# Kernel tuning notes

Measured on AMD Instinct MI355X. Metric: run time of the kernel, lower is better.

Reference implementation:

```python
import jax, jax.numpy as jnp
import numpy as np

DIM = 1024
N_HEAD = 16
N_KV_HEAD = 4
HEAD_DIM = DIM // N_HEAD  # 64
INTER = 2688
B, N = 2, 2048
EPS = 1e-6


def setup_inputs() -> dict:
    key = jax.random.key(0)
    ks = jax.random.split(key, 10)
    std = 0.02
    x = jax.random.normal(ks[0], (B, N, DIM), dtype=jnp.float32)
    # rotary embedding: theta = pos * 10000^(-2i/d), cos/sin of shape [N, HEAD_DIM//2]
    inv_freq = 1.0 / (10000.0 ** (np.arange(0, HEAD_DIM, 2, dtype=np.float32) / HEAD_DIM))
    t = np.arange(N, dtype=np.float32)
    ang = np.outer(t, inv_freq)  # [N, HEAD_DIM//2]
    rope_cos = jnp.asarray(np.cos(ang))
    rope_sin = jnp.asarray(np.sin(ang))
    mask = jnp.tril(jnp.ones((N, N), dtype=bool))  # True = attend
    return {
        "x": x,
        "w_attn_norm": jnp.ones((DIM,), jnp.float32),
        "w_ffn_norm": jnp.ones((DIM,), jnp.float32),
        "Wq": jax.random.normal(ks[1], (DIM, N_HEAD * HEAD_DIM), jnp.float32) * std,
        "Wkv": jax.random.normal(ks[2], (DIM, 2 * N_KV_HEAD * HEAD_DIM), jnp.float32) * std,
        "Wo": jax.random.normal(ks[3], (N_HEAD * HEAD_DIM, DIM), jnp.float32) * std,
        "W1": jax.random.normal(ks[4], (DIM, INTER), jnp.float32) * std,
        "W2": jax.random.normal(ks[5], (INTER, DIM), jnp.float32) * std,
        "W3": jax.random.normal(ks[6], (DIM, INTER), jnp.float32) * std,
        "rope_cos": rope_cos,
        "rope_sin": rope_sin,
        "mask": mask,
    }


def _rms_norm(x, w):
    # nn.functional.rms_norm: x / sqrt(mean(x^2) + eps) * w
    return x * jax.lax.rsqrt(jnp.mean(x * x, axis=-1, keepdims=True) + EPS) * w


def _apply_rope(x, cos, sin):
    # x: [b, n, h, d]; consecutive pairs (x[2k], x[2k+1]) form complex numbers
    xr = x[..., 0::2]
    xi = x[..., 1::2]
    c = cos[None, :, None, :]
    s = sin[None, :, None, :]
    yr = xr * c - xi * s
    yi = xr * s + xi * c
    return jnp.stack([yr, yi], axis=-1).reshape(x.shape)


def _block(x, w_attn_norm, w_ffn_norm, Wq, Wkv, Wo, W1, W2, W3, rope_cos, rope_sin, mask):
    b, n, _ = x.shape
    # --- attention (GQA, use_cache=False prefill) ---
    h = _rms_norm(x, w_attn_norm)
    q = (h @ Wq).reshape(b, n, N_HEAD, HEAD_DIM)
    kv = h @ Wkv
    k, v = jnp.split(kv, 2, axis=-1)
    k = k.reshape(b, n, N_KV_HEAD, HEAD_DIM)
    v = v.reshape(b, n, N_KV_HEAD, HEAD_DIM)
    q = _apply_rope(q, rope_cos, rope_sin)
    k = _apply_rope(k, rope_cos, rope_sin)
    # einops repeat 'b n h d -> b n (r h) d' == tile along head axis
    r = N_HEAD // N_KV_HEAD
    k = jnp.tile(k, (1, 1, r, 1))
    v = jnp.tile(v, (1, 1, r, 1))
    scale = HEAD_DIM ** -0.5
    scores = jnp.einsum('bnhd,bmhd->bhnm', q, k) * scale
    scores = jnp.where(mask[None, None, :, :], scores, jnp.finfo(scores.dtype).min)
    attn = jax.nn.softmax(scores, axis=-1)
    o = jnp.einsum('bhnm,bmhd->bnhd', attn, v).reshape(b, n, N_HEAD * HEAD_DIM)
    x = x + o @ Wo
    # --- SwiGLU MLP ---
    h2 = _rms_norm(x, w_ffn_norm)
    ff = (jax.nn.silu(h2 @ W1) * (h2 @ W3)) @ W2
    return x + ff


def reference(x, w_attn_norm, w_ffn_norm, Wq, Wkv, Wo, W1, W2, W3, rope_cos, rope_sin, mask):
    return _block(x, w_attn_norm, w_ffn_norm, Wq, Wkv, Wo, W1, W2, W3, rope_cos, rope_sin, mask)
```

## Files before the change

kernel.cpp:

```cpp
#include <hip/hip_runtime.h>

#define DIM 1024
#define NH 16
#define NKV 4
#define HD 64
#define INTER 2688
#define BB 2
#define NN 2048
#define MM (BB*NN)

typedef __attribute__((ext_vector_type(4))) float f32x4;
typedef __attribute__((ext_vector_type(16))) float f32x16;
typedef __attribute__((ext_vector_type(8))) short short8;

#define CROW(r,h) ((((r)&3)) + 8*((r)>>2) + 4*(h))

__device__ __forceinline__ unsigned short f2bf(float f) {
  union { float f; unsigned u; } v; v.f = f;
  unsigned r = v.u + 0x7fffu + ((v.u >> 16) & 1u);
  return (unsigned short)(r >> 16);
}

__device__ __forceinline__ void glds16(const unsigned short* g, unsigned short* l) {
  __builtin_amdgcn_global_load_lds(
      (const __attribute__((address_space(1))) void*)g,
      (__attribute__((address_space(3))) void*)l, 16, 0, 0);
}

__global__ void transpose_k(const float* __restrict__ W, unsigned short* __restrict__ Wt,
                            int K, int Nc) {
  __shared__ float tile[32][33];
  int n0 = blockIdx.x * 32, k0 = blockIdx.y * 32;
  int tx = threadIdx.x & 31, ty = threadIdx.x >> 5;
#pragma unroll
  for (int i = 0; i < 32; i += 8)
    tile[ty + i][tx] = W[(size_t)(k0 + ty + i) * Nc + n0 + tx];
  __syncthreads();
#pragma unroll
  for (int i = 0; i < 32; i += 8)
    Wt[(size_t)(n0 + ty + i) * K + k0 + tx] = f2bf(tile[tx][ty + i]);
}

__global__ void rmsnorm_k(const float* __restrict__ x, const float* __restrict__ w,
                          unsigned short* __restrict__ h) {
  int row = blockIdx.x;
  int t = threadIdx.x;
  const float4* xr = (const float4*)(x + (size_t)row * DIM);
  float4 v = xr[t];
  float ss = v.x * v.x + v.y * v.y + v.z * v.z + v.w * v.w;
#pragma unroll
  for (int o = 1; o < 64; o <<= 1) ss += __shfl_xor(ss, o);
  __shared__ float ps[4];
  if ((t & 63) == 0) ps[t >> 6] = ss;
  __syncthreads();
  float r = rsqrtf((ps[0] + ps[1] + ps[2] + ps[3]) * (1.0f / DIM) + 1e-6f);
  const float4* wr = (const float4*)w;
  float4 wv = wr[t];
  ushort4 o4;
  o4.x = f2bf(v.x * r * wv.x);
  o4.y = f2bf(v.y * r * wv.y);
  o4.z = f2bf(v.z * r * wv.z);
  o4.w = f2bf(v.w * r * wv.w);
  *(ushort4*)(h + (size_t)row * DIM + t * 4) = o4;
}

template <bool RES>
__global__ __launch_bounds__(256, 3) void gemm_f32(
    const unsigned short* __restrict__ A, const unsigned short* __restrict__ Bt,
    const float* __restrict__ res, float* __restrict__ C, int Nc, int K) {
  __shared__ __align__(16) unsigned short Asm[2 * 128 * 32];
  __shared__ __align__(16) unsigned short Bsm[2 * 128 * 32];
  int tid = threadIdx.x;
  int w = tid >> 6, l = tid & 63;
  int bm = blockIdx.y * 128, bn = blockIdx.x * 128;
  int wr = (w >> 1) * 64, wc = (w & 1) * 64;
  int c0 = l & 15, g = l >> 4;

  int sr = w * 32 + (l >> 2);
  int sc = ((l & 3) ^ ((sr >> 1) & 3)) * 8;
  const unsigned short* gA0 = A + (size_t)(bm + sr) * K + sc;
  const unsigned short* gA1 = A + (size_t)(bm + sr + 16) * K + sc;
  const unsigned short* gB0 = Bt + (size_t)(bn + sr) * K + sc;
  const unsigned short* gB1 = Bt + (size_t)(bn + sr + 16) * K + sc;
  int ls0 = (w * 32) * 32, ls1 = (w * 32 + 16) * 32;

  int aoff[4], boff[4];
#pragma unroll
  for (int m = 0; m < 4; m++) {
    int ra = wr + m * 16 + c0;
    aoff[m] = ra * 32 + (g ^ ((ra >> 1) & 3)) * 8;
    int rb = wc + m * 16 + c0;
    boff[m] = rb * 32 + (g ^ ((rb >> 1) & 3)) * 8;
  }

  f32x4 acc[4][4] = {};
  int nsteps = K / 32;
  glds16(gA0, &Asm[ls0]);
  glds16(gA1, &Asm[ls1]);
  glds16(gB0, &Bsm[ls0]);
  glds16(gB1, &Bsm[ls1]);
  __syncthreads();
  int buf = 0;
  for (int s = 0; s < nsteps; ++s) {
    int nb = buf ^ 1;
    if (s + 1 < nsteps) {
      int ko = (s + 1) * 32;
      glds16(gA0 + ko, &Asm[nb * 4096 + ls0]);
      glds16(gA1 + ko, &Asm[nb * 4096 + ls1]);
      glds16(gB0 + ko, &Bsm[nb * 4096 + ls0]);
      glds16(gB1 + ko, &Bsm[nb * 4096 + ls1]);
    }
    const unsigned short* As = &Asm[buf * 4096];
    const unsigned short* Bs = &Bsm[buf * 4096];
    short8 af[4], bf[4];
#pragma unroll
    for (int m = 0; m < 4; m++) af[m] = *(const short8*)&As[aoff[m]];
#pragma unroll
    for (int n = 0; n < 4; n++) bf[n] = *(const short8*)&Bs[boff[n]];
#pragma unroll
    for (int m = 0; m < 4; m++)
#pragma unroll
      for (int n = 0; n < 4; n++)
        acc[m][n] = __builtin_amdgcn_mfma_f32_16x16x32_bf16(af[m], bf[n], acc[m][n], 0, 0, 0);
    __syncthreads();
    buf = nb;
  }
  int gq = l >> 4;
#pragma unroll
  for (int m = 0; m < 4; m++) {
#pragma unroll
    for (int i = 0; i < 4; i++) {
      int row = bm + wr + m * 16 + gq * 4 + i;
#pragma unroll
      for (int n = 0; n < 4; n++) {
        int col = bn + wc + n * 16 + c0;
        float v = acc[m][n][i];
        if (RES) v += res[(size_t)row * Nc + col];
        C[(size_t)row * Nc + col] = v;
      }
    }
  }
}

__global__ __launch_bounds__(256, 3) void gemm_ffn13(
    const unsigned short* __restrict__ A, const unsigned short* __restrict__ B1t,
    const unsigned short* __restrict__ B3t, unsigned short* __restrict__ G,
    int Nc, int K) {
  __shared__ __align__(16) unsigned short Asm[2 * 128 * 32];
  __shared__ __align__(16) unsigned short B1sm[2 * 64 * 32];
  __shared__ __align__(16) unsigned short B3sm[2 * 64 * 32];
  int tid = threadIdx.x;
  int w = tid >> 6, l = tid & 63;
  int bm = blockIdx.y * 128, bn = blockIdx.x * 64;
  int wr = (w >> 1) * 64, wc = (w & 1) * 32;
  int c0 = l & 15, g = l >> 4;

  int sr = w * 32 + (l >> 2);
  int sb = w * 16 + (l >> 2);
  int sc  = ((l & 3) ^ ((sr >> 1) & 3)) * 8;
  int scb = ((l & 3) ^ ((sb >> 1) & 3)) * 8;
  const unsigned short* gA0 = A + (size_t)(bm + sr) * K + sc;
  const unsigned short* gA1 = A + (size_t)(bm + sr + 16) * K + sc;
  const unsigned short* gB1 = B1t + (size_t)(bn + sb) * K + scb;
  const unsigned short* gB3 = B3t + (size_t)(bn + sb) * K + scb;
  int ls0 = (w * 32) * 32, ls1 = (w * 32 + 16) * 32, lsb = (w * 16) * 32;

  int aoff[4], boff[2];
#pragma unroll
  for (int m = 0; m < 4; m++) {
    int ra = wr + m * 16 + c0;
    aoff[m] = ra * 32 + (g ^ ((ra >> 1) & 3)) * 8;
  }
#pragma unroll
  for (int n = 0; n < 2; n++) {
    int rb = wc + n * 16 + c0;
    boff[n] = rb * 32 + (g ^ ((rb >> 1) & 3)) * 8;
  }

  f32x4 a1[4][2] = {};
  f32x4 a3[4][2] = {};
  int nsteps = K / 32;
  glds16(gA0, &Asm[ls0]);
  glds16(gA1, &Asm[ls1]);
  glds16(gB1, &B1sm[lsb]);
  glds16(gB3, &B3sm[lsb]);
  __syncthreads();
  int buf = 0;
  for (int s = 0; s < nsteps; ++s) {
    int nb = buf ^ 1;
    if (s + 1 < nsteps) {
      int ko = (s + 1) * 32;
      glds16(gA0 + ko, &Asm[nb * 4096 + ls0]);
      glds16(gA1 + ko, &Asm[nb * 4096 + ls1]);
      glds16(gB1 + ko, &B1sm[nb * 2048 + lsb]);
      glds16(gB3 + ko, &B3sm[nb * 2048 + lsb]);
    }
    const unsigned short* As = &Asm[buf * 4096];
    const unsigned short* B1s = &B1sm[buf * 2048];
    const unsigned short* B3s = &B3sm[buf * 2048];
    short8 af[4], b1f[2], b3f[2];
#pragma unroll
    for (int m = 0; m < 4; m++) af[m] = *(const short8*)&As[aoff[m]];
#pragma unroll
    for (int n = 0; n < 2; n++) {
      b1f[n] = *(const short8*)&B1s[boff[n]];
      b3f[n] = *(const short8*)&B3s[boff[n]];
    }
#pragma unroll
    for (int m = 0; m < 4; m++)
#pragma unroll
      for (int n = 0; n < 2; n++) {
        a1[m][n] = __builtin_amdgcn_mfma_f32_16x16x32_bf16(af[m], b1f[n], a1[m][n], 0, 0, 0);
        a3[m][n] = __builtin_amdgcn_mfma_f32_16x16x32_bf16(af[m], b3f[n], a3[m][n], 0, 0, 0);
      }
    __syncthreads();
    buf = nb;
  }
  int gq = l >> 4;
#pragma unroll
  for (int m = 0; m < 4; m++) {
#pragma unroll
    for (int i = 0; i < 4; i++) {
      int row = bm + wr + m * 16 + gq * 4 + i;
#pragma unroll
      for (int n = 0; n < 2; n++) {
        int col = bn + wc + n * 16 + c0;
        float x1 = a1[m][n][i], x3 = a3[m][n][i];
        float sg = x1 / (1.0f + __expf(-x1));
        G[(size_t)row * Nc + col] = f2bf(sg * x3);
      }
    }
  }
}

__global__ void prep_qkv(const float* __restrict__ qkv, const float* __restrict__ cosb,
                         const float* __restrict__ sinb, unsigned short* __restrict__ qb,
                         unsigned short* __restrict__ kb, unsigned short* __restrict__ vtb) {
  int n = blockIdx.x, b = blockIdx.y;
  int t = threadIdx.x;
  const float* row = qkv + ((size_t)b * NN + n) * 1536;
#pragma unroll
  for (int p = t; p < 512; p += 256) {
    int head = p >> 5, j = p & 31;
    float xr = row[head * 64 + 2 * j], xi = row[head * 64 + 2 * j + 1];
    float c = cosb[n * 32 + j], s = sinb[n * 32 + j];
    size_t o = (((size_t)(b * NH + head)) * NN + n) * 64 + 2 * j;
    qb[o] = f2bf((xr * c - xi * s) * 0.125f);
    qb[o + 1] = f2bf((xr * s + xi * c) * 0.125f);
  }
  if (t < 128) {
    int kvh = t >> 5, j = t & 31;
    float xr = row[1024 + kvh * 64 + 2 * j], xi = row[1024 + kvh * 64 + 2 * j + 1];
    float c = cosb[n * 32 + j], s = sinb[n * 32 + j];
    size_t o = (((size_t)(b * NKV + kvh)) * NN + n) * 64 + 2 * j;
    kb[o] = f2bf(xr * c - xi * s);
    kb[o + 1] = f2bf(xr * s + xi * c);
  }
  {
    int kvh = t >> 6, d = t & 63;
    float v = row[1280 + kvh * 64 + d];
    vtb[(((size_t)(b * NKV + kvh)) * 64 + d) * NN + n] = f2bf(v);
  }
}

__global__ __launch_bounds__(256, 3) void attn_k(
    const unsigned short* __restrict__ qg_, const unsigned short* __restrict__ kg_,
    const unsigned short* __restrict__ vg_, unsigned short* __restrict__ ob) {
  __shared__ __align__(16) unsigned short Ksm[2][64 * 64];
  __shared__ __align__(16) unsigned short Vsm[2][64 * 64];
  int qb = (blockIdx.z == 0) ? (int)blockIdx.x : ((int)gridDim.x - 1 - (int)blockIdx.x);
  int h = blockIdx.y, b = blockIdx.z;
  int kvh = h & 3;
  int tid = threadIdx.x, w = tid >> 6, l = tid & 63;
  int q5 = l & 31, hi = l >> 5;
  int qwbase = qb * 128 + w * 32;
  int qgl = qwbase + q5;

  const unsigned short* Kg = kg_ + ((size_t)(b * NKV + kvh)) * NN * 64;
  const unsigned short* Vg = vg_ + ((size_t)(b * NKV + kvh)) * 64 * NN;

  short8 qf[4];
  {
    const unsigned short* qrow = qg_ + (((size_t)(b * NH + h)) * NN + qgl) * 64 + hi * 8;
#pragma unroll
    for (int d = 0; d < 4; d++) qf[d] = *(const short8*)(qrow + d * 16);
  }

  int srow = l >> 3;
  int schunk = (l & 7) ^ (srow & 7);
  const unsigned short* gK = Kg + (size_t)(w * 16 + srow) * 64 + schunk * 8;
  const unsigned short* gV = Vg + (size_t)(w * 16 + srow) * NN + schunk * 8;

  int nkt = qb * 2 + 2;
  int nkt_w = ((qwbase + 31) >> 6) + 1;

  f32x16 O0 = {}, O1 = {};
  float m_r = -1e30f, l_r = 0.0f;

  glds16(gK, &Ksm[0][w * 1024]);
  glds16(gK + 8 * 64, &Ksm[0][w * 1024 + 512]);
  glds16(gV, &Vsm[0][w * 1024]);
  glds16(gV + 8 * NN, &Vsm[0][w * 1024 + 512]);
  __syncthreads();

  int buf = 0;
  for (int kt = 0; kt < nkt; ++kt) {
    int n0 = kt * 64;
    if (kt + 1 < nkt) {
      int nb = buf ^ 1;
      glds16(gK + (size_t)(n0 + 64) * 64, &Ksm[nb][w * 1024]);
      glds16(gK + (size_t)(n0 + 64) * 64 + 8 * 64, &Ksm[nb][w * 1024 + 512]);
      glds16(gV + n0 + 64, &Vsm[nb][w * 1024]);
      glds16(gV + 8 * NN + n0 + 64, &Vsm[nb][w * 1024 + 512]);
    }
    if (kt < nkt_w) {
      const unsigned short* Ks = Ksm[buf];
      const unsigned short* Vs = Vsm[buf];
      f32x16 S[2];
      __builtin_amdgcn_s_setprio(1);
#pragma unroll
      for (int s = 0; s < 2; s++) {
        f32x16 acc = {};
        int row = s * 32 + q5;
#pragma unroll
        for (int d = 0; d < 4; d++) {
          int ch = (2 * d + hi) ^ (row & 7);
          short8 kf = *(const short8*)&Ks[row * 64 + ch * 8];
          acc = __builtin_amdgcn_mfma_f32_32x32x16_bf16(kf, qf[d], acc, 0, 0, 0);
        }
        S[s] = acc;
      }
      __builtin_amdgcn_s_setprio(0);
      if (kt == nkt_w - 1) {
#pragma unroll
        for (int s = 0; s < 2; s++)
#pragma unroll
          for (int r = 0; r < 16; r++) {
            int kg = n0 + s * 32 + CROW(r, hi);
            S[s][r] = (kg > qgl) ? -1e30f : S[s][r];
          }
      }
      float t[16];
#pragma unroll
      for (int r = 0; r < 16; r++) t[r] = fmaxf(S[0][r], S[1][r]);
#pragma unroll
      for (int k = 8; k >= 1; k >>= 1)
#pragma unroll
        for (int r = 0; r < k; r++) t[r] = fmaxf(t[r], t[r + k]);
      float pm = fmaxf(t[0], __shfl_xor(t[0], 32));
      float mn = fmaxf(m_r, pm);
      float alpha = __expf(m_r - mn);
      m_r = mn;
#pragma unroll
      for (int s = 0; s < 2; s++)
#pragma unroll
        for (int r = 0; r < 16; r++) S[s][r] = __expf(S[s][r] - mn);
      float u[16];
#pragma unroll
      for (int r = 0; r < 16; r++) u[r] = S[0][r] + S[1][r];
#pragma unroll
      for (int k = 8; k >= 1; k >>= 1)
#pragma unroll
        for (int r = 0; r < k; r++) u[r] += u[r + k];
      l_r = l_r * alpha + (u[0] + __shfl_xor(u[0], 32));
      float ab[16];
#pragma unroll
      for (int r = 0; r < 16; r++) ab[r] = __shfl(alpha, CROW(r, 0) + 4 * hi);
#pragma unroll
      for (int r = 0; r < 16; r++) { O0[r] *= ab[r]; O1[r] *= ab[r]; }
      short8 paf[4];
#pragma unroll
      for (int ks = 0; ks < 4; ks++) {
        const int s = ks >> 1, e = ks & 1;
        unsigned a0, a1, b0, b1;
        asm("v_cvt_pk_bf16_f32 %0, %1, %2" : "=v"(a0) : "v"(S[s][8*e+0]), "v"(S[s][8*e+1]));
        asm("v_cvt_pk_bf16_f32 %0, %1, %2" : "=v"(a1) : "v"(S[s][8*e+2]), "v"(S[s][8*e+3]));
        asm("v_cvt_pk_bf16_f32 %0, %1, %2" : "=v"(b0) : "v"(S[s][8*e+4]), "v"(S[s][8*e+5]));
        asm("v_cvt_pk_bf16_f32 %0, %1, %2" : "=v"(b1) : "v"(S[s][8*e+6]), "v"(S[s][8*e+7]));
        asm("v_permlane32_swap_b32 %0, %1" : "+v"(a0), "+v"(b0));
        asm("v_permlane32_swap_b32 %0, %1" : "+v"(a1), "+v"(b1));
        union { unsigned u4[4]; short8 s8; } pk;
        pk.u4[0] = a0; pk.u4[1] = a1; pk.u4[2] = b0; pk.u4[3] = b1;
        paf[ks] = pk.s8;
      }
      __builtin_amdgcn_s_setprio(1);
#pragma unroll
      for (int ks = 0; ks < 4; ks++) {
        int row0 = q5, row1 = 32 + q5;
        short8 vf0 = *(const short8*)&Vs[row0 * 64 + (((2 * ks + hi) ^ (row0 & 7)) * 8)];
        short8 vf1 = *(const short8*)&Vs[row1 * 64 + (((2 * ks + hi) ^ (row1 & 7)) * 8)];
        O0 = __builtin_amdgcn_mfma_f32_32x32x16_bf16(paf[ks], vf0, O0, 0, 0, 0);
        O1 = __builtin_amdgcn_mfma_f32_32x32x16_bf16(paf[ks], vf1, O1, 0, 0, 0);
      }
      __builtin_amdgcn_s_setprio(0);
    }
    __syncthreads();
    buf ^= 1;
  }
  float linv = 1.0f / l_r;
  float lb[16];
#pragma unroll
  for (int r = 0; r < 16; r++) lb[r] = __shfl(linv, CROW(r, 0) + 4 * hi);
#pragma unroll
  for (int r = 0; r < 16; r++) {
    int orow = qwbase + CROW(r, hi);
    size_t base = ((size_t)b * NN + orow) * 1024 + h * 64 + q5;
    ob[base] = f2bf(O0[r] * lb[r]);
    ob[base + 32] = f2bf(O1[r] * lb[r]);
  }
}

extern "C" void kernel_launch(void* const* d_in, const int* in_sizes, int n_in,
                              void* d_out, int out_size, void* d_ws, size_t ws_size,
                              hipStream_t stream) {
  (void)in_sizes; (void)n_in; (void)out_size; (void)ws_size;
  const float* x    = (const float*)d_in[0];
  const float* w_an = (const float*)d_in[1];
  const float* w_fn = (const float*)d_in[2];
  const float* Wq   = (const float*)d_in[3];
  const float* Wkv  = (const float*)d_in[4];
  const float* Wo   = (const float*)d_in[5];
  const float* W1   = (const float*)d_in[6];
  const float* W2   = (const float*)d_in[7];
  const float* W3   = (const float*)d_in[8];
  const float* cosb = (const float*)d_in[9];
  const float* sinb = (const float*)d_in[10];
  float* out = (float*)d_out;

  char* ws = (char*)d_ws;
  size_t off = 0;
  auto take = [&](size_t bytes) {
    size_t r = off;
    off += (bytes + 255) & ~(size_t)255;
    return r;
  };
  unsigned short* WqkvT = (unsigned short*)(ws + take((size_t)1536 * 1024 * 2));
  unsigned short* WoT   = (unsigned short*)(ws + take((size_t)1024 * 1024 * 2));
  unsigned short* W1T   = (unsigned short*)(ws + take((size_t)2688 * 1024 * 2));
  unsigned short* W3T   = (unsigned short*)(ws + take((size_t)2688 * 1024 * 2));
  unsigned short* W2T   = (unsigned short*)(ws + take((size_t)2688 * 1024 * 2));
  unsigned short* hA    = (unsigned short*)(ws + take((size_t)MM * DIM * 2));
  char* qkv_region = ws + take((size_t)MM * 1536 * 4);
  float* qkv = (float*)qkv_region;
  unsigned short* gbuf = (unsigned short*)qkv_region;
  unsigned short* qbuf = (unsigned short*)(ws + take((size_t)MM * DIM * 2));
  unsigned short* kbuf = (unsigned short*)(ws + take((size_t)BB * NKV * NN * HD * 2));
  unsigned short* vtb  = (unsigned short*)(ws + take((size_t)BB * NKV * NN * HD * 2));
  unsigned short* obuf = (unsigned short*)(ws + take((size_t)MM * DIM * 2));
  float* x2 = (float*)(ws + take((size_t)MM * DIM * 4));

  transpose_k<<<dim3(1024 / 32, 1024 / 32), 256, 0, stream>>>(Wq, WqkvT, 1024, 1024);
  transpose_k<<<dim3(512 / 32, 1024 / 32), 256, 0, stream>>>(Wkv, WqkvT + (size_t)1024 * 1024, 1024, 512);
  transpose_k<<<dim3(1024 / 32, 1024 / 32), 256, 0, stream>>>(Wo, WoT, 1024, 1024);
  transpose_k<<<dim3(2688 / 32, 1024 / 32), 256, 0, stream>>>(W1, W1T, 1024, 2688);
  transpose_k<<<dim3(2688 / 32, 1024 / 32), 256, 0, stream>>>(W3, W3T, 1024, 2688);
  transpose_k<<<dim3(1024 / 32, 2688 / 32), 256, 0, stream>>>(W2, W2T, 2688, 1024);

  rmsnorm_k<<<MM, 256, 0, stream>>>(x, w_an, hA);
  gemm_f32<false><<<dim3(1536 / 128, MM / 128), 256, 0, stream>>>(hA, WqkvT, nullptr, qkv, 1536, 1024);
  prep_qkv<<<dim3(NN, BB), 256, 0, stream>>>(qkv, cosb, sinb, qbuf, kbuf, vtb);
  attn_k<<<dim3(NN / 128, NH, BB), 256, 0, stream>>>(qbuf, kbuf, vtb, obuf);
  gemm_f32<true><<<dim3(1024 / 128, MM / 128), 256, 0, stream>>>(obuf, WoT, x, x2, 1024, 1024);
  rmsnorm_k<<<MM, 256, 0, stream>>>(x2, w_fn, hA);
  gemm_ffn13<<<dim3(INTER / 64, MM / 128), 256, 0, stream>>>(hA, W1T, W3T, gbuf, INTER, 1024);
  gemm_f32<true><<<dim3(1024 / 128, MM / 128), 256, 0, stream>>>(gbuf, W2T, x2, out, 1024, 2688);
}
```

Measured before the change: 269.7 us.

## Remap GEMM blocks across XCDs and enlarge FFN13 tile to 256 rows

```diff
diff --git a/kernel.cpp b/kernel.cpp
--- a/kernel.cpp
+++ b/kernel.cpp
@@ -25,6 +25,16 @@
   __builtin_amdgcn_global_load_lds(
       (const __attribute__((address_space(1))) void*)g,
       (__attribute__((address_space(3))) void*)l, 16, 0, 0);
+}
+
+__device__ __forceinline__ void xcd_map(int& bx, int& by) {
+  int gx = gridDim.x;
+  int nwg = gx * gridDim.y;
+  int bid = (int)blockIdx.y * gx + (int)blockIdx.x;
+  int cpx = nwg >> 3;
+  int lg = (bid & 7) * cpx + (bid >> 3);
+  bx = lg % gx;
+  by = lg / gx;
 }
 
 __global__ void transpose_k(const float* __restrict__ W, unsigned short* __restrict__ Wt,
@@ -72,7 +82,9 @@
   __shared__ __align__(16) unsigned short Bsm[2 * 128 * 32];
   int tid = threadIdx.x;
   int w = tid >> 6, l = tid & 63;
-  int bm = blockIdx.y * 128, bn = blockIdx.x * 128;
+  int bx, by;
+  xcd_map(bx, by);
+  int bm = by * 128, bn = bx * 128;
   int wr = (w >> 1) * 64, wc = (w & 1) * 64;
   int c0 = l & 15, g = l >> 4;
 
@@ -142,28 +154,32 @@
   }
 }
 
-__global__ __launch_bounds__(256, 3) void gemm_ffn13(
+__global__ __launch_bounds__(512, 4) void gemm_ffn13(
     const unsigned short* __restrict__ A, const unsigned short* __restrict__ B1t,
     const unsigned short* __restrict__ B3t, unsigned short* __restrict__ G,
     int Nc, int K) {
-  __shared__ __align__(16) unsigned short Asm[2 * 128 * 32];
-  __shared__ __align__(16) unsigned short B1sm[2 * 64 * 32];
-  __shared__ __align__(16) unsigned short B3sm[2 * 64 * 32];
+  __shared__ __align__(16) unsigned short Asm[2][256 * 32];
+  __shared__ __align__(16) unsigned short B1sm[2][64 * 32];
+  __shared__ __align__(16) unsigned short B3sm[2][64 * 32];
   int tid = threadIdx.x;
   int w = tid >> 6, l = tid & 63;
-  int bm = blockIdx.y * 128, bn = blockIdx.x * 64;
+  int bx, by;
+  xcd_map(bx, by);
+  int bm = by * 256, bn = bx * 64;
   int wr = (w >> 1) * 64, wc = (w & 1) * 32;
   int c0 = l & 15, g = l >> 4;
 
-  int sr = w * 32 + (l >> 2);
-  int sb = w * 16 + (l >> 2);
-  int sc  = ((l & 3) ^ ((sr >> 1) & 3)) * 8;
-  int scb = ((l & 3) ^ ((sb >> 1) & 3)) * 8;
-  const unsigned short* gA0 = A + (size_t)(bm + sr) * K + sc;
-  const unsigned short* gA1 = A + (size_t)(bm + sr + 16) * K + sc;
-  const unsigned short* gB1 = B1t + (size_t)(bn + sb) * K + scb;
-  const unsigned short* gB3 = B3t + (size_t)(bn + sb) * K + scb;
-  int ls0 = (w * 32) * 32, ls1 = (w * 32 + 16) * 32, lsb = (w * 16) * 32;
+  int srA = w * 32 + (l >> 2);
+  int srB = (w & 3) * 16 + (l >> 2);
+  int scA = ((l & 3) ^ ((srA >> 1) & 3)) * 8;
+  int scB = ((l & 3) ^ ((srB >> 1) & 3)) * 8;
+  const unsigned short* gA0 = A + (size_t)(bm + srA) * K + scA;
+  const unsigned short* gA1 = A + (size_t)(bm + srA + 16) * K + scA;
+  const unsigned short* gB = (w < 4 ? B1t : B3t) + (size_t)(bn + srB) * K + scB;
+  int lsA0 = (w * 32) * 32, lsA1 = (w * 32 + 16) * 32;
+  int lsB = ((w & 3) * 16) * 32;
+  unsigned short* Bdst0 = (w < 4) ? B1sm[0] : B3sm[0];
+  unsigned short* Bdst1 = (w < 4) ? B1sm[1] : B3sm[1];
 
   int aoff[4], boff[2];
 #pragma unroll
@@ -180,24 +196,22 @@
   f32x4 a1[4][2] = {};
   f32x4 a3[4][2] = {};
   int nsteps = K / 32;
-  glds16(gA0, &Asm[ls0]);
-  glds16(gA1, &Asm[ls1]);
-  glds16(gB1, &B1sm[lsb]);
-  glds16(gB3, &B3sm[lsb]);
+  glds16(gA0, &Asm[0][lsA0]);
+  glds16(gA1, &Asm[0][lsA1]);
+  glds16(gB, Bdst0 + lsB);
   __syncthreads();
   int buf = 0;
   for (int s = 0; s < nsteps; ++s) {
     int nb = buf ^ 1;
     if (s + 1 < nsteps) {
       int ko = (s + 1) * 32;
-      glds16(gA0 + ko, &Asm[nb * 4096 + ls0]);
-      glds16(gA1 + ko, &Asm[nb * 4096 + ls1]);
-      glds16(gB1 + ko, &B1sm[nb * 2048 + lsb]);
-      glds16(gB3 + ko, &B3sm[nb * 2048 + lsb]);
-    }
-    const unsigned short* As = &Asm[buf * 4096];
-    const unsigned short* B1s = &B1sm[buf * 2048];
-    const unsigned short* B3s = &B3sm[buf * 2048];
+      glds16(gA0 + ko, &Asm[nb][lsA0]);
+      glds16(gA1 + ko, &Asm[nb][lsA1]);
+      glds16(gB + ko, (nb ? Bdst1 : Bdst0) + lsB);
+    }
+    const unsigned short* As = Asm[buf];
+    const unsigned short* B1s = B1sm[buf];
+    const unsigned short* B3s = B3sm[buf];
     short8 af[4], b1f[2], b3f[2];
 #pragma unroll
     for (int m = 0; m < 4; m++) af[m] = *(const short8*)&As[aoff[m]];
@@ -462,6 +476,6 @@
   attn_k<<<dim3(NN / 128, NH, BB), 256, 0, stream>>>(qbuf, kbuf, vtb, obuf);
   gemm_f32<true><<<dim3(1024 / 128, MM / 128), 256, 0, stream>>>(obuf, WoT, x, x2, 1024, 1024);
   rmsnorm_k<<<MM, 256, 0, stream>>>(x2, w_fn, hA);
-  gemm_ffn13<<<dim3(INTER / 64, MM / 128), 256, 0, stream>>>(hA, W1T, W3T, gbuf, INTER, 1024);
+  gemm_ffn13<<<dim3(INTER / 64, MM / 256), 512, 0, stream>>>(hA, W1T, W3T, gbuf, INTER, 1024);
   gemm_f32<true><<<dim3(1024 / 128, MM / 128), 256, 0, stream>>>(gbuf, W2T, x2, out, 1024, 2688);
 }
```

Result: no change. 273.7 us (+1.5%).
